# Performance work log

Hardware: AMD Instinct MI355X
Metric: run time of the kernel (lower is better)

The kernel has to match this reference:

```python
import jax, jax.numpy as jnp
import numpy as np
import math

N_LEVELS = 8
PLANE_RES = 512
FEAT_DIM = 16
N_VERT = 10
N_SAMPLES = 262144
LEVEL_OFFSET = 0.0


def _projection_matrices():
    # planotic_solid vertices for n_vertices == 10 (half-dodecahedron)
    phi = (1.0 + math.sqrt(5.0)) / 2.0
    verts = np.array([
        [1.0, 1.0, 1.0], [1.0, 1.0, -1.0], [1.0, -1.0, 1.0], [1.0, -1.0, -1.0],
        [0.0, phi, 1.0 / phi], [0.0, phi, -1.0 / phi],
        [1.0 / phi, 0.0, phi], [1.0 / phi, 0.0, -phi],
        [phi, 1.0 / phi, 0.0], [phi, -1.0 / phi, 0.0]], dtype=np.float64)
    verts /= np.linalg.norm(verts, axis=-1, keepdims=True)
    Ps = []
    for a in verts:
        if a[0] != 0 or a[1] != 0:
            p0 = np.array([-a[1], a[0], 0.0])
        else:
            p0 = np.array([0.0, -a[2], a[1]])
        p1 = np.cross(a, p0)
        p0 /= np.linalg.norm(p0)
        p1 /= np.linalg.norm(p1)
        Ps.append(np.stack([p0, p1], axis=0))
    return np.stack(Ps, axis=0).astype(np.float32)  # (V, 2, 3)

P_MATS = _projection_matrices()

# static ripmap geometry: plane (l1, l2) has shape (H = res>>l2, W = res>>l1)
_W = np.array([PLANE_RES >> l for l in range(N_LEVELS)], dtype=np.int32)
_H = _W.copy()
_SIZES = np.array([int(_H[l2]) * int(_W[l1])
                   for l1 in range(N_LEVELS) for l2 in range(N_LEVELS)], dtype=np.int64)
_OFFS = np.concatenate([[0], np.cumsum(_SIZES)[:-1]]).astype(np.int32)


def build_ripmaps_flat(fm):
    """Build the 8x8 anisotropic mip pyramid and pack all planes into one flat buffer.
    fm: (V, H, W, F). Returns (V, total_pixels, F)."""
    flats = []
    base = fm
    for l1 in range(N_LEVELS):
        if l1 > 0:
            base = 0.5 * (base[:, :, 0::2] + base[:, :, 1::2])  # AvgPool (1,2): pool width
        cur = base
        for l2 in range(N_LEVELS):
            if l2 > 0:
                cur = 0.5 * (cur[:, 0::2] + cur[:, 1::2])        # AvgPool (2,1): pool height
            flats.append(cur.reshape(N_VERT, -1, FEAT_DIM))
    return jnp.concatenate(flats, axis=1)


def multi_anisomip_interp(flat, coords, level):
    """flat: (V, T, F) packed ripmaps; coords: (N, V, 2) in [-1, 1];
    level: (N, V, 2) fractional levels in [0, L-1].
    Quadrilinear: bilinear in space x bilinear across the (l1, l2) level grid."""
    W_arr = jnp.asarray(_W)
    H_arr = jnp.asarray(_H)
    off_arr = jnp.asarray(_OFFS)
    vidx = jnp.arange(N_VERT)[None, :]
    lx, ly = level[..., 0], level[..., 1]
    l1f_f = jnp.clip(jnp.floor(lx), 0.0, N_LEVELS - 1)
    l2f_f = jnp.clip(jnp.floor(ly), 0.0, N_LEVELS - 1)
    wx = jnp.clip(lx - l1f_f, 0.0, 1.0)
    wy = jnp.clip(ly - l2f_f, 0.0, 1.0)
    l1f = l1f_f.astype(jnp.int32)
    l2f = l2f_f.astype(jnp.int32)
    l1c = jnp.minimum(l1f + 1, N_LEVELS - 1)
    l2c = jnp.minimum(l2f + 1, N_LEVELS - 1)
    enc = jnp.zeros(coords.shape[:-1] + (FEAT_DIM,), dtype=flat.dtype)
    for l1, wl1 in ((l1f, 1.0 - wx), (l1c, wx)):
        Wl = W_arr[l1]  # (N, V)
        for l2, wl2 in ((l2f, 1.0 - wy), (l2c, wy)):
            Hl = H_arr[l2]
            off = off_arr[l1 * N_LEVELS + l2]
            u = (coords[..., 0] * 0.5 + 0.5) * Wl - 0.5
            v = (coords[..., 1] * 0.5 + 0.5) * Hl - 0.5
            uf = jnp.floor(u)
            vf = jnp.floor(v)
            fu = u - uf
            fv = v - vf
            ix0 = jnp.clip(uf.astype(jnp.int32), 0, Wl - 1)
            ix1 = jnp.clip(uf.astype(jnp.int32) + 1, 0, Wl - 1)
            iy0 = jnp.clip(vf.astype(jnp.int32), 0, Hl - 1)
            iy1 = jnp.clip(vf.astype(jnp.int32) + 1, 0, Hl - 1)
            wl = wl1 * wl2
            for ix, iy, wc in ((ix0, iy0, (1 - fu) * (1 - fv)),
                               (ix1, iy0, fu * (1 - fv)),
                               (ix0, iy1, (1 - fu) * fv),
                               (ix1, iy1, fu * fv)):
                idx = off + iy * Wl + ix  # (N, V) flat pixel index
                enc = enc + (wl * wc)[..., None] * flat[vidx, idx]
    return enc  # (N, V, F)


def setup_inputs() -> dict:
    key = jax.random.key(0)
    k1, k2, k3 = jax.random.split(key, 3)
    means = jax.random.uniform(k1, (N_SAMPLES, 3), minval=-1.0, maxval=1.0, dtype=jnp.float32)
    A = jax.random.normal(k2, (N_SAMPLES, 3, 3), dtype=jnp.float32) * 0.02
    covs = jnp.einsum('nij,nkj->nik', A, A) + 1e-10 * jnp.eye(3, dtype=jnp.float32)
    fm = jax.random.uniform(k3, (N_VERT, PLANE_RES, PLANE_RES, FEAT_DIM),
                            minval=-0.01, maxval=0.01, dtype=jnp.float32)
    return {"means": means, "covs": covs, "fm": fm}


def reference(means, covs, fm):
    P = jnp.asarray(P_MATS)                                   # (V, 2, 3)
    means_proj = jnp.einsum('nd,vcd->nvc', means, P)          # (N, V, 2)
    sig2 = jnp.einsum('vad,nde,vae->nva', P, covs, P)         # diag of P C P^T, (N, V, 2)
    sigmas = jnp.sqrt(jnp.maximum(sig2, 1e-20))
    level = jnp.log2(sigmas) + LEVEL_OFFSET + math.log2(PLANE_RES)
    level = jnp.clip(level, 0.0, N_LEVELS - 1)
    flat = build_ripmaps_flat(fm)
    enc = multi_anisomip_interp(flat, means_proj, level)      # (N, V, F)
    return enc.reshape(means.shape[0], N_VERT * FEAT_DIM)
```

## Files before the change

kernel.cpp:

```cpp
#include <hip/hip_runtime.h>
#include <hip/hip_fp16.h>


#define NV 10
#define FD 16
#define NS 262144
#define PYR_PX 1040400L
#define PYR_BYTES 332928000L

__constant__ float c_P[NV][2][3] = {
  {{-0.7071067811865476f, 0.7071067811865476f, 0.0f},
   {-0.4082482904638631f,-0.4082482904638631f, 0.8164965809277261f}},
  {{-0.7071067811865476f, 0.7071067811865476f, 0.0f},
   { 0.4082482904638631f, 0.4082482904638631f, 0.8164965809277261f}},
  {{ 0.7071067811865476f, 0.7071067811865476f, 0.0f},
   {-0.4082482904638631f, 0.4082482904638631f, 0.8164965809277261f}},
  {{ 0.7071067811865476f, 0.7071067811865476f, 0.0f},
   { 0.4082482904638631f,-0.4082482904638631f, 0.8164965809277261f}},
  {{-1.0f, 0.0f, 0.0f},
   { 0.0f,-0.3568220897730899f, 0.9341723589627157f}},
  {{-1.0f, 0.0f, 0.0f},
   { 0.0f, 0.3568220897730899f, 0.9341723589627157f}},
  {{ 0.0f, 1.0f, 0.0f},
   {-0.9341723589627157f, 0.0f, 0.3568220897730899f}},
  {{ 0.0f, 1.0f, 0.0f},
   { 0.9341723589627157f, 0.0f, 0.3568220897730899f}},
  {{-0.3568220897730899f, 0.9341723589627157f, 0.0f},
   { 0.0f, 0.0f, 1.0f}},
  {{ 0.3568220897730899f, 0.9341723589627157f, 0.0f},
   { 0.0f, 0.0f, 1.0f}},
};

__constant__ int c_CW[8] = {0, 512, 768, 896, 960, 992, 1008, 1016};

__device__ __forceinline__ int offp_a(int l1, int l2) {
  return 1044480 - (1020 << (10 - l1)) + ((1024 - (1024 >> l2)) << (9 - l1));
}

__device__ __forceinline__ uint4 havg(uint4 a, uint4 c, __half2 hhalf) {
  uint4 res;
  __half2* rr = (__half2*)&res;
  const __half2* ha = (const __half2*)&a;
  const __half2* hc = (const __half2*)&c;
  #pragma unroll
  for (int j = 0; j < 4; ++j) rr[j] = __hmul2(__hadd2(ha[j], hc[j]), hhalf);
  return res;
}

__global__ __launch_bounds__(256) void build_all(const float* __restrict__ fm,
                                                 __half* __restrict__ pyr)
{
  __shared__ uint4 ldsA[2048];
  __shared__ uint4 ldsB[1024];
  int bid = blockIdx.x;
  int v = bid >> 8;
  int rem = bid & 255;
  int b = rem >> 2;
  int s = rem & 3;
  int t = threadIdx.x;

  __half* bv = pyr + (long)v * PYR_PX * FD;
  uint4* bv4 = (uint4*)bv;
  const __half2 hhalf = __floats2half2_rn(0.5f, 0.5f);

  {
    const float4* src = (const float4*)(fm +
        (((long)v * 512 + b * 8) * 512 + s * 128) * FD);
    uint2* ldsu2 = (uint2*)ldsA;
    uint2* g0 = (uint2*)bv;
    #pragma unroll
    for (int i = 0; i < 16; ++i) {
      int u = t + 256 * i;
      int r = u >> 9;
      int f4 = u & 511;
      int px = f4 >> 2, q = f4 & 3;
      float4 d = src[(long)r * 2048 + f4];
      __half2 h0 = __floats2half2_rn(d.x, d.y);
      __half2 h1 = __floats2half2_rn(d.z, d.w);
      uint2 val;
      val.x = *(unsigned*)&h0; val.y = *(unsigned*)&h1;
      ldsu2[(r * 128 + px) * 4 + q] = val;
      g0[((long)(b * 8 + r) * 512 + s * 128 + px) * 4 + q] = val;
    }
  }
  __syncthreads();

  #pragma unroll
  for (int l1 = 0; l1 < 8; ++l1) {
    uint4* cur = (l1 & 1) ? ldsB : ldsA;
    const int Wc = 128 >> l1;

    if (l1 < 7) {
      uint4* nxt = (l1 & 1) ? ldsA : ldsB;
      const int Wn = Wc >> 1;
      const int units = 8 * Wn * 2;
      const int Wgn = 512 >> (l1 + 1);
      const int colbase = offp_a(l1 + 1, 0) + s * Wn;
      for (int u = t; u < units; u += 256) {
        int k = u & 1;
        int xr = u >> 1;
        int x = xr & (Wn - 1);
        int r = xr >> (6 - l1);
        uint4 a = cur[(r * Wc + 2 * x) * 2 + k];
        uint4 c = cur[(r * Wc + 2 * x + 1) * 2 + k];
        uint4 res = havg(a, c, hhalf);
        nxt[(r * Wn + x) * 2 + k] = res;
        bv4[(long)(colbase + (b * 8 + r) * Wgn + x) * 2 + k] = res;
      }
    }

    {
      const int slots = Wc * 2;
      if (t < slots) {
        int k = t & 1, x = t >> 1;
        const int Wg = 512 >> l1;
        uint4 r0 = cur[(0 * Wc + x) * 2 + k];
        uint4 r1 = cur[(1 * Wc + x) * 2 + k];
        uint4 r2 = cur[(2 * Wc + x) * 2 + k];
        uint4 r3 = cur[(3 * Wc + x) * 2 + k];
        uint4 r4 = cur[(4 * Wc + x) * 2 + k];
        uint4 r5 = cur[(5 * Wc + x) * 2 + k];
        uint4 r6 = cur[(6 * Wc + x) * 2 + k];
        uint4 r7 = cur[(7 * Wc + x) * 2 + k];
        uint4 a0 = havg(r0, r1, hhalf), a1 = havg(r2, r3, hhalf);
        uint4 a2 = havg(r4, r5, hhalf), a3 = havg(r6, r7, hhalf);
        uint4 b0 = havg(a0, a1, hhalf), b1 = havg(a2, a3, hhalf);
        uint4 c0 = havg(b0, b1, hhalf);
        int gx = s * Wc + x;
        long p1 = (long)offp_a(l1, 1) + (long)(b * 4) * Wg + gx;
        bv4[p1 * 2 + k] = a0;
        bv4[(p1 + Wg) * 2 + k] = a1;
        bv4[(p1 + 2 * Wg) * 2 + k] = a2;
        bv4[(p1 + 3 * Wg) * 2 + k] = a3;
        long p2 = (long)offp_a(l1, 2) + (long)(b * 2) * Wg + gx;
        bv4[p2 * 2 + k] = b0;
        bv4[(p2 + Wg) * 2 + k] = b1;
        long p3 = (long)offp_a(l1, 3) + (long)b * Wg + gx;
        bv4[p3 * 2 + k] = c0;
      }
    }
    __syncthreads();
  }
}

template<int L2SRC, int NLEV>
__global__ __launch_bounds__(256) void pool_hN(__half* __restrict__ pyr)
{
  constexpr int R = 1 << NLEV;
  constexpr int HL = 512 >> (L2SRC + NLEV);
  int total = NV * HL * 2040;
  int t = blockIdx.x * 256 + threadIdx.x;
  if (t >= total) return;
  int u = t % 2040;
  int r2 = t / 2040;
  int c = u >> 1, k = u & 1;
  int y = r2 % HL;
  int v = r2 / HL;
  int l1 = 0;
  #pragma unroll
  for (int i = 1; i < 8; ++i) l1 += (c >= c_CW[i]) ? 1 : 0;
  int x = c - c_CW[l1];
  int W = 512 >> l1;
  __half* bv = pyr + (long)v * PYR_PX * FD;
  const __half* src = bv + (long)offp_a(l1, L2SRC) * FD;

  uint4 d[R];
  long base = ((long)(y * R) * W + x) * FD + k * 8;
  #pragma unroll
  for (int r = 0; r < R; ++r)
    d[r] = *(const uint4*)(src + base + (long)r * W * FD);

  const __half2 hhalf = __floats2half2_rn(0.5f, 0.5f);
  #pragma unroll
  for (int lev = 1; lev <= NLEV; ++lev) {
    int cnt = R >> lev;
    __half* dst = bv + (long)offp_a(l1, L2SRC + lev) * FD;
    #pragma unroll
    for (int r = 0; r < cnt; ++r) {
      d[r] = havg(d[2 * r], d[2 * r + 1], hhalf);
      *(uint4*)(dst + (((long)(y * cnt + r)) * W + x) * FD + k * 8) = d[r];
    }
  }
}

__global__ __launch_bounds__(256) void proj_kernel(const float* __restrict__ means,
                                                   const float* __restrict__ covs,
                                                   float4* __restrict__ pl)
{
  int n = blockIdx.x * 256 + threadIdx.x;
  if (n >= NS) return;
  float m0 = means[3 * n], m1 = means[3 * n + 1], m2 = means[3 * n + 2];
  const float* C = covs + 9L * n;
  float c0 = C[0], c1 = C[1], c2 = C[2];
  float c3 = C[3], c4 = C[4], c5 = C[5];
  float c6 = C[6], c7 = C[7], c8 = C[8];
  #pragma unroll
  for (int v = 0; v < NV; ++v) {
    float p00 = c_P[v][0][0], p01 = c_P[v][0][1], p02 = c_P[v][0][2];
    float p10 = c_P[v][1][0], p11 = c_P[v][1][1], p12 = c_P[v][1][2];
    float cx = m0 * p00 + m1 * p01 + m2 * p02;
    float cy = m0 * p10 + m1 * p11 + m2 * p12;
    float t0 = c0 * p00 + c1 * p01 + c2 * p02;
    float t1 = c3 * p00 + c4 * p01 + c5 * p02;
    float t2 = c6 * p00 + c7 * p01 + c8 * p02;
    float s2x = p00 * t0 + p01 * t1 + p02 * t2;
    t0 = c0 * p10 + c1 * p11 + c2 * p12;
    t1 = c3 * p10 + c4 * p11 + c5 * p12;
    t2 = c6 * p10 + c7 * p11 + c8 * p12;
    float s2y = p10 * t0 + p11 * t1 + p12 * t2;
    float lx = 0.5f * log2f(fmaxf(s2x, 1e-20f)) + 9.0f;
    float ly = 0.5f * log2f(fmaxf(s2y, 1e-20f)) + 9.0f;
    lx = fminf(fmaxf(lx, 0.0f), 7.0f);
    ly = fminf(fmaxf(ly, 0.0f), 7.0f);
    pl[(long)v * NS + n] = make_float4(cx, cy, lx, ly);
  }
}

__global__ __launch_bounds__(256) void interp6(const float4* __restrict__ pl,
                                               const __half* __restrict__ pyr,
                                               float* __restrict__ out)
{
  int bid = blockIdx.x;
  int swz = (bid & 7) * 5120 + (bid >> 3);
  int t = swz * 256 + threadIdx.x;
  int q = t & 3;
  int vlow = (t >> 2) & 1;
  int n = (t >> 3) & (NS - 1);
  int v2 = t >> 21;
  int v = v2 * 2 + vlow;

  float4 p = pl[(long)v * NS + n];
  float cx = p.x, cy = p.y, lx = p.z, ly = p.w;
  int l1f = (int)lx, l2f = (int)ly;
  float wx = lx - (float)l1f, wy = ly - (float)l2f;
  int l1c = min(l1f + 1, 7);
  int l2c = min(l2f + 1, 7);

  bool qodd = (q & 1);

  int sh_0 = 9 - l1f;
  int Ar_0 = 1044480 - (1020 << (10 - l1f));
  float u0 = (cx * 0.5f + 0.5f) * (float)(1 << sh_0) - 0.5f;
  float uf0 = floorf(u0);
  float fu0 = u0 - uf0;
  int iu0 = (int)uf0;
  bool e0 = (iu0 < 0) || (iu0 >= (1 << sh_0) - 1);
  int ix_0 = min(max(iu0, 0), (1 << sh_0) - 1);
  float wxl_0 = qodd ? (e0 ? 0.0f : fu0) : (e0 ? 1.0f : 1.0f - fu0);
  int sh_1 = 9 - l1c;
  int Ar_1 = 1044480 - (1020 << (10 - l1c));
  float u1 = (cx * 0.5f + 0.5f) * (float)(1 << sh_1) - 0.5f;
  float uf1 = floorf(u1);
  float fu1 = u1 - uf1;
  int iu1 = (int)uf1;
  bool e1 = (iu1 < 0) || (iu1 >= (1 << sh_1) - 1);
  int ix_1 = min(max(iu1, 0), (1 << sh_1) - 1);
  float wxl_1 = qodd ? (e1 ? 0.0f : fu1) : (e1 ? 1.0f : 1.0f - fu1);

  float wl1_0 = 1.0f - wx, wl1_1 = wx;

  int H0 = 512 >> l2f;
  float vv0 = (cy * 0.5f + 0.5f) * (float)H0 - 0.5f;
  float vf0 = floorf(vv0);
  float fv_0 = vv0 - vf0;
  int iv0 = (int)vf0;
  int iy_0 = min(max(iv0, 0), H0 - 1);
  int dy_0 = min(max(iv0 + 1, 0), H0 - 1) - iy_0;
  int Bv_0 = 1024 - (1024 >> l2f);

  int H1 = 512 >> l2c;
  float vv1 = (cy * 0.5f + 0.5f) * (float)H1 - 0.5f;
  float vf1 = floorf(vv1);
  float fv_1 = vv1 - vf1;
  int iv1 = (int)vf1;
  int iy_1 = min(max(iv1, 0), H1 - 1);
  int dy_1 = min(max(iv1 + 1, 0), H1 - 1) - iy_1;
  int Bv_1 = 1024 - (1024 >> l2c);

  float wl2_0 = 1.0f - wy, wl2_1 = wy;

  int oA = Ar_0 + ((Bv_0 + iy_0) << sh_0) + ix_0;
  int oB = oA + (dy_0 << sh_0);
  int oC = Ar_0 + ((Bv_1 + iy_1) << sh_0) + ix_0;
  int oD = oC + (dy_1 << sh_0);
  int oE = Ar_1 + ((Bv_0 + iy_0) << sh_1) + ix_1;
  int oF = oE + (dy_0 << sh_1);
  int oG = Ar_1 + ((Bv_1 + iy_1) << sh_1) + ix_1;
  int oH = oG + (dy_1 << sh_1);

  float wb00 = wl1_0 * wl2_0 * wxl_0;
  float wb01 = wl1_0 * wl2_1 * wxl_0;
  float wb10 = wl1_1 * wl2_0 * wxl_1;
  float wb11 = wl1_1 * wl2_1 * wxl_1;
  __half2 wA = __float2half2_rn(wb00 * (1.0f - fv_0));
  __half2 wB = __float2half2_rn(wb00 * fv_0);
  __half2 wC = __float2half2_rn(wb01 * (1.0f - fv_1));
  __half2 wD = __float2half2_rn(wb01 * fv_1);
  __half2 wE = __float2half2_rn(wb10 * (1.0f - fv_0));
  __half2 wF = __float2half2_rn(wb10 * fv_0);
  __half2 wG = __float2half2_rn(wb11 * (1.0f - fv_1));
  __half2 wH = __float2half2_rn(wb11 * fv_1);

  const __half* bvq = pyr + (long)v * PYR_PX * FD + ((q & 1) * 16 + (q >> 1) * 8);

  uint4 dA = *(const uint4*)(bvq + (long)oA * FD);
  uint4 dB = *(const uint4*)(bvq + (long)oB * FD);
  uint4 dC = *(const uint4*)(bvq + (long)oC * FD);
  uint4 dD = *(const uint4*)(bvq + (long)oD * FD);
  uint4 dE = *(const uint4*)(bvq + (long)oE * FD);
  uint4 dF = *(const uint4*)(bvq + (long)oF * FD);
  uint4 dG = *(const uint4*)(bvq + (long)oG * FD);
  uint4 dH = *(const uint4*)(bvq + (long)oH * FD);
  __builtin_amdgcn_sched_barrier(0);

  __half2 z = __float2half2_rn(0.0f);
  __half2 acc0 = z, acc1 = z, acc2 = z, acc3 = z;
  #define ACC8(D, W) { const __half2* hh = (const __half2*)&(D);      \
    acc0 = __hfma2(hh[0], (W), acc0); acc1 = __hfma2(hh[1], (W), acc1); \
    acc2 = __hfma2(hh[2], (W), acc2); acc3 = __hfma2(hh[3], (W), acc3); }
  ACC8(dA, wA) ACC8(dB, wB) ACC8(dC, wC) ACC8(dD, wD)
  ACC8(dE, wE) ACC8(dF, wF) ACC8(dG, wG) ACC8(dH, wH)
  #undef ACC8

  int a0 = *(int*)&acc0, a1 = *(int*)&acc1;
  int a2 = *(int*)&acc2, a3 = *(int*)&acc3;
  int b0 = __shfl_xor(a0, 1), b1 = __shfl_xor(a1, 1);
  int b2 = __shfl_xor(a2, 1), b3 = __shfl_xor(a3, 1);
  acc0 = __hadd2(acc0, *(__half2*)&b0);
  acc1 = __hadd2(acc1, *(__half2*)&b1);
  acc2 = __hadd2(acc2, *(__half2*)&b2);
  acc3 = __hadd2(acc3, *(__half2*)&b3);

  __half2 s0 = qodd ? acc2 : acc0;
  __half2 s1 = qodd ? acc3 : acc1;
  float2 f0 = __half22float2(s0);
  float2 f1 = __half22float2(s1);
  *(float4*)(out + ((long)n * NV + v) * FD + q * 4) =
      make_float4(f0.x, f0.y, f1.x, f1.y);
}

extern "C" void kernel_launch(void* const* d_in, const int* in_sizes, int n_in,
                              void* d_out, int out_size, void* d_ws, size_t ws_size,
                              hipStream_t stream)
{
  const float* means = (const float*)d_in[0];
  const float* covs  = (const float*)d_in[1];
  const float* fm    = (const float*)d_in[2];
  float* out = (float*)d_out;
  __half* pyr = (__half*)d_ws;
  float4* pl  = (float4*)((char*)d_ws + PYR_BYTES);

  build_all<<<NV * 256, 256, 0, stream>>>(fm, pyr);
  {
    int tB = NV * 8 * 2040;
    pool_hN<3, 3><<<(tB + 255) / 256, 256, 0, stream>>>(pyr);
    int tC = NV * 4 * 2040;
    pool_hN<6, 1><<<(tC + 255) / 256, 256, 0, stream>>>(pyr);
  }
  proj_kernel<<<(NS + 255) / 256, 256, 0, stream>>>(means, covs, pl);

  interp6<<<40960, 256, 0, stream>>>(pl, pyr, out);
}
```

Baseline: 273.6 us.

## Add shifted duplicate planes so odd-x bilinear taps read aligned pixel pairs

Adds a build_dup kernel that writes shifted copies of the mid-level ripmap planes (levels 2-5 on both axes), each pixel paired with its right neighbour. The interp kernel now reads from these duplicate planes when the left tap index is odd. The aim is for the two horizontal taps to fall in an aligned pair, so each fetch is more coalesced or hits fewer cache lines. This costs an extra pyramid build pass, more workspace memory and extra address logic in the interpolation kernel.

```diff
diff --git a/kernel.cpp b/kernel.cpp
--- a/kernel.cpp
+++ b/kernel.cpp
@@ -7,6 +7,9 @@
 #define NS 262144
 #define PYR_PX 1040400L
 #define PYR_BYTES 332928000L
+#define DUP0_PX 10404000
+#define DUP_VPX 57600
+#define OFF_PL 351360000L
 
 __constant__ float c_P[NV][2][3] = {
   {{-0.7071067811865476f, 0.7071067811865476f, 0.0f},
@@ -183,6 +186,29 @@
   }
 }
 
+__global__ __launch_bounds__(256) void build_dup(__half* __restrict__ pyr)
+{
+  int cb = blockIdx.y;
+  int l1 = 2 + (cb >> 2), l2 = 2 + (cb & 3);
+  int W = 512 >> l1, H = 512 >> l2;
+  int units = NV * W * H * 2;
+  int gx = blockIdx.x * 256 + threadIdx.x;
+  if (gx >= units) return;
+  int k = gx & 1;
+  int p = gx >> 1;
+  int x = p & (W - 1);
+  int r = p >> (9 - l1);
+  int y = r & (H - 1);
+  int v = r >> (9 - l2);
+  long srcPx = (long)v * PYR_PX + offp_a(l1, l2) + y * W + min(x + 1, W - 1);
+  int Ad = 61440 - (245760 >> l1);
+  int Bd = 256 - (1024 >> l2);
+  long dstPx = (long)DUP0_PX + (long)v * DUP_VPX + Ad + ((Bd + y) << (9 - l1)) + x;
+  const uint4* src = (const uint4*)(pyr + srcPx * FD);
+  uint4* dst = (uint4*)(pyr + dstPx * FD);
+  dst[k] = src[k];
+}
+
 __global__ __launch_bounds__(256) void proj_kernel(const float* __restrict__ means,
                                                    const float* __restrict__ covs,
                                                    float4* __restrict__ pl)
@@ -216,7 +242,7 @@
   }
 }
 
-__global__ __launch_bounds__(256) void interp6(const float4* __restrict__ pl,
+__global__ __launch_bounds__(256) void interp7(const float4* __restrict__ pl,
                                                const __half* __restrict__ pyr,
                                                float* __restrict__ out)
 {
@@ -237,6 +263,7 @@
   int l2c = min(l2f + 1, 7);
 
   bool qodd = (q & 1);
+  int dupRel = DUP0_PX + v * DUP_VPX - v * 1040400;
 
   int sh_0 = 9 - l1f;
   int Ar_0 = 1044480 - (1020 << (10 - l1f));
@@ -247,6 +274,10 @@
   bool e0 = (iu0 < 0) || (iu0 >= (1 << sh_0) - 1);
   int ix_0 = min(max(iu0, 0), (1 << sh_0) - 1);
   float wxl_0 = qodd ? (e0 ? 0.0f : fu0) : (e0 ? 1.0f : 1.0f - fu0);
+  int pOdd_0 = ix_0 & 1;
+  int Ad_0 = 61440 - (245760 >> l1f);
+  int inR1_0 = ((unsigned)(l1f - 2) <= 3u) ? 1 : 0;
+
   int sh_1 = 9 - l1c;
   int Ar_1 = 1044480 - (1020 << (10 - l1c));
   float u1 = (cx * 0.5f + 0.5f) * (float)(1 << sh_1) - 0.5f;
@@ -256,6 +287,9 @@
   bool e1 = (iu1 < 0) || (iu1 >= (1 << sh_1) - 1);
   int ix_1 = min(max(iu1, 0), (1 << sh_1) - 1);
   float wxl_1 = qodd ? (e1 ? 0.0f : fu1) : (e1 ? 1.0f : 1.0f - fu1);
+  int pOdd_1 = ix_1 & 1;
+  int Ad_1 = 61440 - (245760 >> l1c);
+  int inR1_1 = ((unsigned)(l1c - 2) <= 3u) ? 1 : 0;
 
   float wl1_0 = 1.0f - wx, wl1_1 = wx;
 
@@ -267,6 +301,8 @@
   int iy_0 = min(max(iv0, 0), H0 - 1);
   int dy_0 = min(max(iv0 + 1, 0), H0 - 1) - iy_0;
   int Bv_0 = 1024 - (1024 >> l2f);
+  int Bd_0 = 256 - (1024 >> l2f);
+  int inR2_0 = ((unsigned)(l2f - 2) <= 3u) ? 1 : 0;
 
   int H1 = 512 >> l2c;
   float vv1 = (cy * 0.5f + 0.5f) * (float)H1 - 0.5f;
@@ -276,16 +312,26 @@
   int iy_1 = min(max(iv1, 0), H1 - 1);
   int dy_1 = min(max(iv1 + 1, 0), H1 - 1) - iy_1;
   int Bv_1 = 1024 - (1024 >> l2c);
+  int Bd_1 = 256 - (1024 >> l2c);
+  int inR2_1 = ((unsigned)(l2c - 2) <= 3u) ? 1 : 0;
 
   float wl2_0 = 1.0f - wy, wl2_1 = wy;
 
-  int oA = Ar_0 + ((Bv_0 + iy_0) << sh_0) + ix_0;
+  bool s00 = pOdd_0 && inR1_0 && inR2_0;
+  int oA = s00 ? (dupRel + Ad_0 + ((Bd_0 + iy_0) << sh_0) + ix_0 - 1)
+               : (Ar_0 + ((Bv_0 + iy_0) << sh_0) + ix_0);
   int oB = oA + (dy_0 << sh_0);
-  int oC = Ar_0 + ((Bv_1 + iy_1) << sh_0) + ix_0;
+  bool s01 = pOdd_0 && inR1_0 && inR2_1;
+  int oC = s01 ? (dupRel + Ad_0 + ((Bd_1 + iy_1) << sh_0) + ix_0 - 1)
+               : (Ar_0 + ((Bv_1 + iy_1) << sh_0) + ix_0);
   int oD = oC + (dy_1 << sh_0);
-  int oE = Ar_1 + ((Bv_0 + iy_0) << sh_1) + ix_1;
+  bool s10 = pOdd_1 && inR1_1 && inR2_0;
+  int oE = s10 ? (dupRel + Ad_1 + ((Bd_0 + iy_0) << sh_1) + ix_1 - 1)
+               : (Ar_1 + ((Bv_0 + iy_0) << sh_1) + ix_1);
   int oF = oE + (dy_0 << sh_1);
-  int oG = Ar_1 + ((Bv_1 + iy_1) << sh_1) + ix_1;
+  bool s11 = pOdd_1 && inR1_1 && inR2_1;
+  int oG = s11 ? (dupRel + Ad_1 + ((Bd_1 + iy_1) << sh_1) + ix_1 - 1)
+               : (Ar_1 + ((Bv_1 + iy_1) << sh_1) + ix_1);
   int oH = oG + (dy_1 << sh_1);
 
   float wb00 = wl1_0 * wl2_0 * wxl_0;
@@ -348,7 +394,7 @@
   const float* fm    = (const float*)d_in[2];
   float* out = (float*)d_out;
   __half* pyr = (__half*)d_ws;
-  float4* pl  = (float4*)((char*)d_ws + PYR_BYTES);
+  float4* pl  = (float4*)((char*)d_ws + OFF_PL);
 
   build_all<<<NV * 256, 256, 0, stream>>>(fm, pyr);
   {
@@ -357,7 +403,11 @@
     int tC = NV * 4 * 2040;
     pool_hN<6, 1><<<(tC + 255) / 256, 256, 0, stream>>>(pyr);
   }
+  {
+    dim3 g(1280, 16, 1);
+    build_dup<<<g, 256, 0, stream>>>(pyr);
+  }
   proj_kernel<<<(NS + 255) / 256, 256, 0, stream>>>(means, covs, pl);
 
-  interp6<<<40960, 256, 0, stream>>>(pl, pyr, out);
-}
+  interp7<<<40960, 256, 0, stream>>>(pl, pyr, out);
+}
```

After: 271.2 us. About the same (-0.9%).
